# Kernel optimization log

Measured on AMD Instinct MI355X. Metric: run time of the kernel, lower is better.

Reference implementation:

```python
import jax, jax.numpy as jnp
import numpy as np
import math

B, S, D, H = 4, 1024, 1024, 16
HD = D // H
R = 128  # max_rel_pos
EPS = 1e-5

def setup_inputs() -> dict:
    key = jax.random.key(0)
    ks = jax.random.split(key, 20)
    sd = 1.0 / math.sqrt(D)
    def lin(k, din, dout):
        return jax.random.normal(k, (din, dout), jnp.float32) * (1.0 / math.sqrt(din))
    return {
        "x": jax.random.normal(ks[0], (B, S, D), jnp.float32),
        "wq": lin(ks[1], D, D), "bq": jnp.zeros((D,), jnp.float32),
        "wk": lin(ks[2], D, D), "bk": jnp.zeros((D,), jnp.float32),
        "wv": lin(ks[3], D, D), "bv": jnp.zeros((D,), jnp.float32),
        "wo": lin(ks[4], D, D), "bo": jnp.zeros((D,), jnp.float32),
        "rel_embed": jax.random.normal(ks[5], (2 * R + 1, HD), jnp.float32),
        "ln1_g": jnp.ones((D,), jnp.float32), "ln1_b": jnp.zeros((D,), jnp.float32),
        "ln2_g": jnp.ones((D,), jnp.float32), "ln2_b": jnp.zeros((D,), jnp.float32),
        "w1": lin(ks[6], D, 4 * D), "b1": jnp.zeros((4 * D,), jnp.float32),
        "w2": lin(ks[7], 4 * D, D), "b2": jnp.zeros((D,), jnp.float32),
    }

def _layernorm(x, g, b):
    mu = jnp.mean(x, axis=-1, keepdims=True)
    var = jnp.mean(jnp.square(x - mu), axis=-1, keepdims=True)
    return (x - mu) * jax.lax.rsqrt(var + EPS) * g + b

def _block(x, wq, bq, wk, bk, wv, bv, wo, bo, rel_embed,
           ln1_g, ln1_b, ln2_g, ln2_b, w1, b1, w2, b2):
    h = _layernorm(x, ln1_g, ln1_b)
    # project and split heads: [B,S,D] -> [B,H,S,HD]
    def heads(y):
        return y.reshape(B, S, H, HD).transpose(0, 2, 1, 3)
    Q = heads(h @ wq + bq)
    K = heads(h @ wk + bk)
    V = heads(h @ wv + bv)
    scale = 1.0 / math.sqrt(HD)
    scores = jnp.einsum("bhqd,bhkd->bhqk", Q, K) * scale
    # relative positions: clamp(q-k, -R, R) + R
    pos = jnp.arange(S)
    rel_idx = jnp.clip(pos[None, :] - pos[:, None], -R, R) + R  # [S,S]
    rel = rel_embed[rel_idx]  # [S,S,HD]
    scores = scores + jnp.einsum("bhqd,qkd->bhqk", Q, rel) * scale
    attn = jax.nn.softmax(scores, axis=-1)
    out = jnp.einsum("bhqk,bhkd->bhqd", attn, V)
    out = out.transpose(0, 2, 1, 3).reshape(B, S, D) @ wo + bo
    x = x + out  # dropout is identity in eval
    h2 = _layernorm(x, ln2_g, ln2_b)
    ff = jax.nn.gelu(h2 @ w1 + b1, approximate=False) @ w2 + b2
    return x + ff

def reference(x, wq, bq, wk, bk, wv, bv, wo, bo, rel_embed,
              ln1_g, ln1_b, ln2_g, ln2_b, w1, b1, w2, b2):
    return _block(x, wq, bq, wk, bk, wv, bv, wo, bo, rel_embed,
                  ln1_g, ln1_b, ln2_g, ln2_b, w1, b1, w2, b2)
```

## Files before the change

### kernel.cpp

```cpp
#include <hip/hip_runtime.h>

typedef unsigned short u16;
typedef __bf16 bf16x8 __attribute__((ext_vector_type(8)));
typedef float f32x4 __attribute__((ext_vector_type(4)));

#define QSCALE 0.18033688011112042f
#define QREL_LD 320

__device__ __forceinline__ float b2f(u16 x) {
    unsigned int u = ((unsigned int)x) << 16;
    return __builtin_bit_cast(float, u);
}
__device__ __forceinline__ u16 f2bf(float f) {
    unsigned int u = __builtin_bit_cast(unsigned int, f);
    u += 0x7fffu + ((u >> 16) & 1u);
    return (u16)(u >> 16);
}
__device__ __forceinline__ void lds_load16(const u16* g, u16* l) {
    __builtin_amdgcn_global_load_lds(
        (const __attribute__((address_space(1))) void*)g,
        (__attribute__((address_space(3))) void*)l, 16, 0, 0);
}

__global__ void transpose_f32_bf16(const float* __restrict__ in, u16* __restrict__ out,
                                   int R, int C) {
    __shared__ u16 tile[32][33];
    int bx = blockIdx.x * 32, by = blockIdx.y * 32;
    int tx = threadIdx.x, ty = threadIdx.y;
#pragma unroll
    for (int i = 0; i < 32; i += 8)
        tile[ty + i][tx] = f2bf(in[(size_t)(by + ty + i) * C + bx + tx]);
    __syncthreads();
#pragma unroll
    for (int i = 0; i < 32; i += 8)
        out[(size_t)(bx + ty + i) * R + by + tx] = tile[tx][ty + i];
}

__global__ void transpose_w4(const float* __restrict__ wq, const float* __restrict__ wk,
                             const float* __restrict__ wv, const float* __restrict__ wo,
                             u16* __restrict__ wqkvT, u16* __restrict__ woT) {
    __shared__ u16 tile[32][33];
    int z = blockIdx.z;
    const float* in = (z == 0) ? wq : (z == 1) ? wk : (z == 2) ? wv : wo;
    u16* out = (z < 3) ? (wqkvT + (size_t)z * 1024 * 1024) : woT;
    int bx = blockIdx.x * 32, by = blockIdx.y * 32;
    int tx = threadIdx.x, ty = threadIdx.y;
#pragma unroll
    for (int i = 0; i < 32; i += 8)
        tile[ty + i][tx] = f2bf(in[(size_t)(by + ty + i) * 1024 + bx + tx]);
    __syncthreads();
#pragma unroll
    for (int i = 0; i < 32; i += 8)
        out[(size_t)(bx + ty + i) * 1024 + by + tx] = tile[tx][ty + i];
}

__global__ void transpose_v(const u16* __restrict__ in, int ldin, int coloff,
                            u16* __restrict__ out) {
    __shared__ u16 tile[32][33];
    size_t zout = (size_t)blockIdx.z << 20;
    int bx = blockIdx.x * 32, by = blockIdx.y * 32;
    int tx = threadIdx.x, ty = threadIdx.y;
#pragma unroll
    for (int i = 0; i < 32; i += 8)
        tile[ty + i][tx] =
            in[(size_t)(blockIdx.z * 1024 + by + ty + i) * ldin + coloff + bx + tx];
    __syncthreads();
#pragma unroll
    for (int i = 0; i < 32; i += 8)
        out[zout + (size_t)(bx + ty + i) * 1024 + by + tx] = tile[tx][ty + i];
}

__global__ void cvt_f32_bf16(const float* __restrict__ in, u16* __restrict__ out, int n) {
    int i = blockIdx.x * 256 + threadIdx.x;
    if (i < n) out[i] = f2bf(in[i]);
}

__global__ void fill_f32(float* __restrict__ p, float v, int n) {
    int i = blockIdx.x * 256 + threadIdx.x;
    if (i < n) p[i] = v;
}

__global__ void concat3(const float* a, const float* b, const float* c, float* o) {
    int i = blockIdx.x * 256 + threadIdx.x;
    o[i] = (i < 1024) ? a[i] : (i < 2048 ? b[i - 1024] : c[i - 2048]);
}

__global__ __launch_bounds__(256) void ln_kernel(
    const u16* __restrict__ inb, const float* __restrict__ inf,
    const float* __restrict__ g, const float* __restrict__ b,
    u16* __restrict__ out) {
    int row = blockIdx.x, t = threadIdx.x;
    size_t base = (size_t)row * 1024 + t * 4;
    float v[4];
    if (inf) {
        float4 f = *(const float4*)(inf + base);
        v[0] = f.x; v[1] = f.y; v[2] = f.z; v[3] = f.w;
    } else {
        uint2 u = *(const uint2*)(inb + base);
        v[0] = b2f((u16)(u.x & 0xffff)); v[1] = b2f((u16)(u.x >> 16));
        v[2] = b2f((u16)(u.y & 0xffff)); v[3] = b2f((u16)(u.y >> 16));
    }
    float s = v[0] + v[1] + v[2] + v[3];
    float q = v[0] * v[0] + v[1] * v[1] + v[2] * v[2] + v[3] * v[3];
#pragma unroll
    for (int m = 1; m < 64; m <<= 1) {
        s += __shfl_xor(s, m);
        q += __shfl_xor(q, m);
    }
    __shared__ float rs[4], rq[4];
    __shared__ float mu_s, rstd_s;
    int w = t >> 6, lane = t & 63;
    if (lane == 0) { rs[w] = s; rq[w] = q; }
    __syncthreads();
    if (t == 0) {
        float S = rs[0] + rs[1] + rs[2] + rs[3];
        float Q2 = rq[0] + rq[1] + rq[2] + rq[3];
        float mu = S * (1.0f / 1024.0f);
        float var = Q2 * (1.0f / 1024.0f) - mu * mu;
        mu_s = mu;
        rstd_s = rsqrtf(var + 1e-5f);
    }
    __syncthreads();
    float mu = mu_s, rstd = rstd_s;
    u16 o[4];
#pragma unroll
    for (int i = 0; i < 4; i++) {
        int col = t * 4 + i;
        o[i] = f2bf((v[i] - mu) * rstd * g[col] + b[col]);
    }
    uint2 pk;
    pk.x = (unsigned)o[0] | ((unsigned)o[1] << 16);
    pk.y = (unsigned)o[2] | ((unsigned)o[3] << 16);
    *(uint2*)(out + base) = pk;
}

template <int BN>
__global__ __launch_bounds__(256) void gemm_bt(
    const u16* __restrict__ A, int lda, long long sAz,
    const u16* __restrict__ Bt, int ldb, long long sBz, int nclamp,
    const float* __restrict__ bias,
    const float* __restrict__ resid_f32,
    u16* __restrict__ outb, float* __restrict__ outf, int ldc, long long sCz,
    int K, float oscale, int gelu) {
    constexpr int NJ = BN / 32;
    constexpr int NUNITS = 8 + BN / 16;
    constexpr int UPW = NUNITS / 4;
    __shared__ __align__(16) u16 As[2][128 * 32];
    __shared__ __align__(16) u16 Bs[2][BN * 32];
    int t = threadIdx.x, w = t >> 6, lane = t & 63;
    int z = blockIdx.z;
    const u16* Ab = A + (size_t)z * sAz;
    const u16* Bb = Bt + (size_t)z * sBz;
    int m0 = blockIdx.y * 128, n0 = blockIdx.x * BN;
    int lo = lane & 15, hi = lane >> 4;
    int wr = w >> 1, wc = w & 1;
    f32x4 acc[4][NJ];
#pragma unroll
    for (int i = 0; i < 4; i++)
#pragma unroll
        for (int j = 0; j < NJ; j++) acc[i][j] = (f32x4){0.f, 0.f, 0.f, 0.f};

    auto stage = [&](int k0, int buf) {
#pragma unroll
        for (int uu = 0; uu < UPW; ++uu) {
            int u = w * UPW + uu;
            if (u < 8) {
                int s = u * 64 + lane;
                int row = s >> 2, c8 = (s & 3) * 8;
                const u16* gp = Ab + (size_t)(m0 + row) * lda + k0 + c8;
                lds_load16(gp, &As[buf][u * 512]);
            } else {
                int s = (u - 8) * 64 + lane;
                int row = s >> 2, c8 = (s & 3) * 8;
                int n = n0 + row;
                if (n >= nclamp) n = nclamp - 1;
                const u16* gp = Bb + (size_t)n * ldb + k0 + c8;
                lds_load16(gp, &Bs[buf][(u - 8) * 512]);
            }
        }
    };

    int nk = K >> 5;
    stage(0, 0);
    for (int kk = 0; kk < nk; ++kk) {
        __syncthreads();
        if (kk + 1 < nk) stage((kk + 1) << 5, (kk + 1) & 1);
        int buf = kk & 1;
        bf16x8 a[4], bb[NJ];
#pragma unroll
        for (int i = 0; i < 4; i++)
            a[i] = *(const bf16x8*)&As[buf][(wr * 64 + i * 16 + lo) * 32 + 8 * hi];
#pragma unroll
        for (int j = 0; j < NJ; j++)
            bb[j] = *(const bf16x8*)&Bs[buf][(wc * (BN / 2) + j * 16 + lo) * 32 + 8 * hi];
#pragma unroll
        for (int i = 0; i < 4; i++)
#pragma unroll
            for (int j = 0; j < NJ; j++)
                acc[i][j] = __builtin_amdgcn_mfma_f32_16x16x32_bf16(a[i], bb[j], acc[i][j], 0, 0, 0);
    }
#pragma unroll
    for (int j = 0; j < NJ; j++) {
        int col = n0 + wc * (BN / 2) + j * 16 + lo;
        float bv = bias ? bias[col] : 0.f;
#pragma unroll
        for (int i = 0; i < 4; i++) {
            int rbase = m0 + wr * 64 + i * 16 + hi * 4;
#pragma unroll
            for (int r = 0; r < 4; r++) {
                float v = fmaf(acc[i][j][r], oscale, bv);
                if (gelu) v = 0.5f * v * (1.f + erff(v * 0.70710678118654752f));
                size_t ridx = (size_t)(rbase + r) * ldc + col;
                if (resid_f32) v += resid_f32[ridx];
                size_t idx = (size_t)z * sCz + ridx;
                if (outf) outf[idx] = v;
                if (outb) outb[idx] = f2bf(v);
            }
        }
    }
}

__global__ __launch_bounds__(256) void gemm_bt64(
    const u16* __restrict__ A, int lda,
    const u16* __restrict__ Bt, int ldb,
    const float* __restrict__ bias,
    const float* __restrict__ resid_f32, const u16* __restrict__ resid_bf,
    u16* __restrict__ outb, float* __restrict__ outf, int ldc,
    int K, float oscale, int gelu) {
    constexpr int AU = 16, BU = 8, UPW = (AU + BU) / 4;
    __shared__ __align__(16) u16 As[2][128 * 64];
    __shared__ __align__(16) u16 Bs[2][64 * 64];
    int t = threadIdx.x, w = t >> 6, lane = t & 63;
    int m0 = blockIdx.y * 128, n0 = blockIdx.x * 64;
    int lo = lane & 15, hi = lane >> 4;
    int wr = w >> 1, wc = w & 1;
    f32x4 acc[4][2];
#pragma unroll
    for (int i = 0; i < 4; i++)
#pragma unroll
        for (int j = 0; j < 2; j++) acc[i][j] = (f32x4){0.f, 0.f, 0.f, 0.f};

    auto stage = [&](int k0, int buf) {
#pragma unroll
        for (int uu = 0; uu < UPW; ++uu) {
            int u = w * UPW + uu;
            if (u < AU) {
                int s = u * 64 + lane;
                int row = s >> 3, cg = (lane & 7) ^ (row & 7);
                lds_load16(A + (size_t)(m0 + row) * lda + k0 + cg * 8,
                           &As[buf][u * 512]);
            } else {
                int u2 = u - AU;
                int s = u2 * 64 + lane;
                int row = s >> 3, cg = (lane & 7) ^ (row & 7);
                lds_load16(Bt + (size_t)(n0 + row) * ldb + k0 + cg * 8,
                           &Bs[buf][u2 * 512]);
            }
        }
    };

    int nk = K >> 6;
    stage(0, 0);
    for (int kk = 0; kk < nk; ++kk) {
        __syncthreads();
        if (kk + 1 < nk) stage((kk + 1) << 6, (kk + 1) & 1);
        int buf = kk & 1;
#pragma unroll
        for (int k2 = 0; k2 < 2; ++k2) {
            bf16x8 a[4], bb[2];
#pragma unroll
            for (int i = 0; i < 4; i++) {
                int row = wr * 64 + i * 16 + lo;
                int g = (k2 * 4 + hi) ^ (row & 7);
                a[i] = *(const bf16x8*)&As[buf][row * 64 + g * 8];
            }
#pragma unroll
            for (int j = 0; j < 2; j++) {
                int row = wc * 32 + j * 16 + lo;
                int g = (k2 * 4 + hi) ^ (row & 7);
                bb[j] = *(const bf16x8*)&Bs[buf][row * 64 + g * 8];
            }
#pragma unroll
            for (int i = 0; i < 4; i++)
#pragma unroll
                for (int j = 0; j < 2; j++)
                    acc[i][j] = __builtin_amdgcn_mfma_f32_16x16x32_bf16(a[i], bb[j], acc[i][j], 0, 0, 0);
        }
    }
#pragma unroll
    for (int j = 0; j < 2; j++) {
        int col = n0 + wc * 32 + j * 16 + lo;
        float bv = bias ? bias[col] : 0.f;
#pragma unroll
        for (int i = 0; i < 4; i++) {
            int rbase = m0 + wr * 64 + i * 16 + hi * 4;
#pragma unroll
            for (int r = 0; r < 4; r++) {
                float v = fmaf(acc[i][j][r], oscale, bv);
                if (gelu) v = 0.5f * v * (1.f + erff(v * 0.70710678118654752f));
                size_t ridx = (size_t)(rbase + r) * ldc + col;
                if (resid_f32) v += resid_f32[ridx];
                if (resid_bf) v += b2f(resid_bf[ridx]);
                if (outf) outf[ridx] = v;
                if (outb) outb[ridx] = f2bf(v);
            }
        }
    }
}

__global__ __launch_bounds__(256) void gemm_bt128k64(
    const u16* __restrict__ A, int lda,
    const u16* __restrict__ Bt, int ldb,
    const float* __restrict__ bias,
    u16* __restrict__ outb, int ldc,
    int K, float oscale, int gelu) {
    __shared__ __align__(16) u16 As[2][128 * 64];
    __shared__ __align__(16) u16 Bs[2][128 * 64];
    int t = threadIdx.x, w = t >> 6, lane = t & 63;
    int m0 = blockIdx.y * 128, n0 = blockIdx.x * 128;
    int lo = lane & 15, hi = lane >> 4;
    int wr = w >> 1, wc = w & 1;
    f32x4 acc[4][4];
#pragma unroll
    for (int i = 0; i < 4; i++)
#pragma unroll
        for (int j = 0; j < 4; j++) acc[i][j] = (f32x4){0.f, 0.f, 0.f, 0.f};

    auto stage = [&](int k0, int buf) {
#pragma unroll
        for (int uu = 0; uu < 4; ++uu) {
            int u = w * 4 + uu;
            int s = u * 64 + lane;
            int row = s >> 3, cg = (lane & 7) ^ (row & 7);
            lds_load16(A + (size_t)(m0 + row) * lda + k0 + cg * 8,
                       &As[buf][u * 512]);
        }
#pragma unroll
        for (int uu = 0; uu < 4; ++uu) {
            int u = w * 4 + uu;
            int s = u * 64 + lane;
            int row = s >> 3, cg = (lane & 7) ^ (row & 7);
            lds_load16(Bt + (size_t)(n0 + row) * ldb + k0 + cg * 8,
                       &Bs[buf][u * 512]);
        }
    };

    int nk = K >> 6;
    stage(0, 0);
    for (int kk = 0; kk < nk; ++kk) {
        __syncthreads();
        if (kk + 1 < nk) stage((kk + 1) << 6, (kk + 1) & 1);
        int buf = kk & 1;
#pragma unroll
        for (int k2 = 0; k2 < 2; ++k2) {
            bf16x8 a[4], bb[4];
#pragma unroll
            for (int i = 0; i < 4; i++) {
                int row = wr * 64 + i * 16 + lo;
                int g = (k2 * 4 + hi) ^ (row & 7);
                a[i] = *(const bf16x8*)&As[buf][row * 64 + g * 8];
            }
#pragma unroll
            for (int j = 0; j < 4; j++) {
                int row = wc * 64 + j * 16 + lo;
                int g = (k2 * 4 + hi) ^ (row & 7);
                bb[j] = *(const bf16x8*)&Bs[buf][row * 64 + g * 8];
            }
#pragma unroll
            for (int i = 0; i < 4; i++)
#pragma unroll
                for (int j = 0; j < 4; j++)
                    acc[i][j] = __builtin_amdgcn_mfma_f32_16x16x32_bf16(a[i], bb[j], acc[i][j], 0, 0, 0);
        }
    }
#pragma unroll
    for (int j = 0; j < 4; j++) {
        int col = n0 + wc * 64 + j * 16 + lo;
        float bv = bias ? bias[col] : 0.f;
#pragma unroll
        for (int i = 0; i < 4; i++) {
            int rbase = m0 + wr * 64 + i * 16 + hi * 4;
#pragma unroll
            for (int r = 0; r < 4; r++) {
                float v = fmaf(acc[i][j][r], oscale, bv);
                if (gelu) v = 0.5f * v * (1.f + erff(v * 0.70710678118654752f));
                outb[(size_t)(rbase + r) * ldc + col] = f2bf(v);
            }
        }
    }
}

__global__ __launch_bounds__(256) void attn_kernel(
    const u16* __restrict__ QKV, const u16* __restrict__ Vtg,
    const u16* __restrict__ Qrel, u16* __restrict__ Ob) {
    __shared__ __align__(16) u16 KsL[2][4096];
    __shared__ __align__(16) u16 VsL[2][4096];
    __shared__ __align__(16) u16 Ps[4][16 * 72];
    int t = threadIdx.x, w = t >> 6, lane = t & 63;
    int bid = blockIdx.x;
    int qblk = bid & 15, h = (bid >> 4) & 15, bb = bid >> 8;
    int lo = lane & 15, hi = lane >> 4;
    int q0b = qblk * 64;
    int q0 = q0b + w * 16;

    const u16* qrow = QKV + ((size_t)(bb * 1024 + q0 + lo) * 3072 + h * 64 + hi * 8);
    bf16x8 qf0 = *(const bf16x8*)qrow;
    bf16x8 qf1 = *(const bf16x8*)(qrow + 32);

    const size_t qrel_base = (size_t)h * (4096ull * QREL_LD);
    float blo[4], bhi[4];
#pragma unroll
    for (int r = 0; r < 4; r++) {
        size_t row = qrel_base + (size_t)(bb * 1024 + q0 + hi * 4 + r) * QREL_LD;
        blo[r] = b2f(Qrel[row]);
        bhi[r] = b2f(Qrel[row + 256]);
    }

    const u16* Kg = QKV + 1024 + ((size_t)(bb * 1024)) * 3072 + h * 64;
    const u16* Vg = Vtg + ((size_t)(bb * 1024 + h * 64)) * 1024;

    auto stage = [&](int k0, int buf) {
#pragma unroll
        for (int half = 0; half < 2; ++half) {
            int s = half * 256 + w * 64 + lane;
            int row = s >> 3, cg = (s & 7) ^ (row & 7);
            lds_load16(Kg + (size_t)(k0 + row) * 3072 + cg * 8,
                       &KsL[buf][(half * 256 + w * 64) * 8]);
            lds_load16(Vg + (size_t)row * 1024 + k0 + cg * 8,
                       &VsL[buf][(half * 256 + w * 64) * 8]);
        }
    };

    f32x4 oacc[4];
#pragma unroll
    for (int j = 0; j < 4; j++) oacc[j] = (f32x4){0.f, 0.f, 0.f, 0.f};
    float l_[4] = {0.f, 0.f, 0.f, 0.f};

    stage(0, 0);
    for (int c = 0; c < 16; ++c) {
        int k0 = c * 64;
        __syncthreads();
        if (c < 15) stage(k0 + 64, (c + 1) & 1);
        const u16* Ksb = KsL[c & 1];
        const u16* Vsb = VsL[c & 1];

        f32x4 sc[4];
#pragma unroll
        for (int kt = 0; kt < 4; kt++) {
            int row = kt * 16 + lo, rx = row & 7;
            bf16x8 kf0 = *(const bf16x8*)&Ksb[(row * 8 + (hi ^ rx)) * 8];
            bf16x8 kf1 = *(const bf16x8*)&Ksb[(row * 8 + ((4 + hi) ^ rx)) * 8];
            f32x4 zz = (f32x4){0.f, 0.f, 0.f, 0.f};
            sc[kt] = __builtin_amdgcn_mfma_f32_16x16x32_bf16(qf0, kf0, zz, 0, 0, 0);
            sc[kt] = __builtin_amdgcn_mfma_f32_16x16x32_bf16(qf1, kf1, sc[kt], 0, 0, 0);
        }
        float bt[4][4];
        if (k0 + 192 <= q0b) {
#pragma unroll
            for (int kt = 0; kt < 4; kt++)
#pragma unroll
                for (int r = 0; r < 4; r++) bt[kt][r] = blo[r];
        } else if (k0 >= q0b + 192) {
#pragma unroll
            for (int kt = 0; kt < 4; kt++)
#pragma unroll
                for (int r = 0; r < 4; r++) bt[kt][r] = bhi[r];
        } else {
#pragma unroll
            for (int kt = 0; kt < 4; kt++)
#pragma unroll
                for (int r = 0; r < 4; r++) {
                    int q = q0 + hi * 4 + r;
                    int k = k0 + kt * 16 + lo;
                    int p = k - q;
                    p = p < -128 ? -128 : (p > 128 ? 128 : p);
                    p += 128;
                    bt[kt][r] = b2f(Qrel[qrel_base + (size_t)(bb * 1024 + q) * QREL_LD + p]);
                }
        }
#pragma unroll
        for (int kt = 0; kt < 4; kt++)
#pragma unroll
            for (int r = 0; r < 4; r++) {
                float s = fmaf(sc[kt][r], QSCALE, bt[kt][r]);
                float p = __builtin_amdgcn_exp2f(s);
                l_[r] += p;
                Ps[w][(hi * 4 + r) * 72 + kt * 16 + lo] =
                    (u16)(__builtin_bit_cast(unsigned int, p) >> 16);
            }
        bf16x8 pf0 = *(const bf16x8*)&Ps[w][lo * 72 + 8 * hi];
        bf16x8 pf1 = *(const bf16x8*)&Ps[w][lo * 72 + 32 + 8 * hi];
#pragma unroll
        for (int j = 0; j < 4; j++) {
            int row = j * 16 + lo, rx = row & 7;
            bf16x8 vf0 = *(const bf16x8*)&Vsb[(row * 8 + (hi ^ rx)) * 8];
            bf16x8 vf1 = *(const bf16x8*)&Vsb[(row * 8 + ((4 + hi) ^ rx)) * 8];
            oacc[j] = __builtin_amdgcn_mfma_f32_16x16x32_bf16(pf0, vf0, oacc[j], 0, 0, 0);
            oacc[j] = __builtin_amdgcn_mfma_f32_16x16x32_bf16(pf1, vf1, oacc[j], 0, 0, 0);
        }
    }
#pragma unroll
    for (int r = 0; r < 4; r++) {
#pragma unroll
        for (int m = 1; m < 16; m <<= 1) l_[r] += __shfl_xor(l_[r], m);
    }
#pragma unroll
    for (int r = 0; r < 4; r++) {
        float inv = 1.f / l_[r];
        int q = q0 + hi * 4 + r;
#pragma unroll
        for (int j = 0; j < 4; j++)
            Ob[(size_t)(bb * 1024 + q) * 1024 + h * 64 + j * 16 + lo] =
                f2bf(oacc[j][r] * inv);
    }
}

extern "C" void kernel_launch(void* const* d_in, const int* in_sizes, int n_in,
                              void* d_out, int out_size, void* d_ws, size_t ws_size,
                              hipStream_t stream) {
    const float* x   = (const float*)d_in[0];
    const float* wq  = (const float*)d_in[1];
    const float* bq  = (const float*)d_in[2];
    const float* wk  = (const float*)d_in[3];
    const float* bk  = (const float*)d_in[4];
    const float* wv  = (const float*)d_in[5];
    const float* bv  = (const float*)d_in[6];
    const float* wo  = (const float*)d_in[7];
    const float* bo  = (const float*)d_in[8];
    const float* rel = (const float*)d_in[9];
    const float* g1  = (const float*)d_in[10];
    const float* be1 = (const float*)d_in[11];
    const float* g2  = (const float*)d_in[12];
    const float* be2 = (const float*)d_in[13];
    const float* w1  = (const float*)d_in[14];
    const float* bf1 = (const float*)d_in[15];
    const float* w2  = (const float*)d_in[16];
    const float* bf2 = (const float*)d_in[17];

    char* ws = (char*)d_ws;
    const size_t MB = 1024ull * 1024ull;
    u16* wqkvT = (u16*)(ws + 0 * MB);
    u16* woT  = (u16*)(ws + 6 * MB);
    u16* w1T  = (u16*)(ws + 8 * MB);
    u16* w2T  = (u16*)(ws + 16 * MB);
    u16* h    = (u16*)(ws + 24 * MB);
    u16* QKV  = (u16*)(ws + 32 * MB);
    u16* Vtg  = (u16*)(ws + 56 * MB);
    u16* qrel = (u16*)(ws + 64 * MB);
    u16* x2b  = (u16*)(ws + 64 * MB);
    u16* att  = (u16*)(ws + 112 * MB);
    u16* relb = (u16*)(ws + 120 * MB);
    float* cbias = (float*)(ws + 120 * MB + 64 * 1024);
    float* bqkv  = (float*)(ws + 120 * MB + 128 * 1024);
    u16* ff1  = (u16*)(ws + 32 * MB);
    u16* h2   = h;

    dim3 tb(32, 8);
    transpose_w4<<<dim3(32, 32, 4), tb, 0, stream>>>(wq, wk, wv, wo, wqkvT, woT);
    transpose_f32_bf16<<<dim3(128, 32), tb, 0, stream>>>(w1, w1T, 1024, 4096);
    transpose_f32_bf16<<<dim3(32, 128), tb, 0, stream>>>(w2, w2T, 4096, 1024);
    cvt_f32_bf16<<<65, 256, 0, stream>>>(rel, relb, 257 * 64);
    fill_f32<<<2, 256, 0, stream>>>(cbias, -16.0f, QREL_LD);
    concat3<<<12, 256, 0, stream>>>(bq, bk, bv, bqkv);

    ln_kernel<<<4096, 256, 0, stream>>>(nullptr, x, g1, be1, h);

    gemm_bt128k64<<<dim3(24, 32), 256, 0, stream>>>(h, 1024, wqkvT, 1024,
        bqkv, QKV, 3072, 1024, 1.f, 0);
    transpose_v<<<dim3(32, 32, 4), tb, 0, stream>>>(QKV, 3072, 2048, Vtg);

    gemm_bt<64><<<dim3(5, 32, 16), 256, 0, stream>>>(QKV, 3072, 64, relb, 64, 0, 257,
        cbias, nullptr, qrel, nullptr, QREL_LD, (long long)4096 * QREL_LD,
        64, QSCALE, 0);

    attn_kernel<<<1024, 256, 0, stream>>>(QKV, Vtg, qrel, att);

    gemm_bt64<<<dim3(16, 32), 256, 0, stream>>>(att, 1024, woT, 1024,
        bo, x, nullptr, x2b, nullptr, 1024, 1024, 1.f, 0);

    ln_kernel<<<4096, 256, 0, stream>>>(x2b, nullptr, g2, be2, h2);

    gemm_bt128k64<<<dim3(32, 32), 256, 0, stream>>>(h2, 1024, w1T, 1024,
        bf1, ff1, 4096, 1024, 1.f, 1);
    gemm_bt64<<<dim3(16, 32), 256, 0, stream>>>(ff1, 4096, w2T, 4096,
        bf2, nullptr, x2b, nullptr, (float*)d_out, 1024, 4096, 1.f, 0);
}
```

Measured before the change: 419.8 us.

## Fuse Q·rel_embed projection into attention kernel via per-warp LDS table

```diff
diff --git a/kernel.cpp b/kernel.cpp
--- a/kernel.cpp
+++ b/kernel.cpp
@@ -5,7 +5,6 @@
 typedef float f32x4 __attribute__((ext_vector_type(4)));
 
 #define QSCALE 0.18033688011112042f
-#define QREL_LD 320
 
 __device__ __forceinline__ float b2f(u16 x) {
     unsigned int u = ((unsigned int)x) << 16;
@@ -73,11 +72,6 @@
 __global__ void cvt_f32_bf16(const float* __restrict__ in, u16* __restrict__ out, int n) {
     int i = blockIdx.x * 256 + threadIdx.x;
     if (i < n) out[i] = f2bf(in[i]);
-}
-
-__global__ void fill_f32(float* __restrict__ p, float v, int n) {
-    int i = blockIdx.x * 256 + threadIdx.x;
-    if (i < n) p[i] = v;
 }
 
 __global__ void concat3(const float* a, const float* b, const float* c, float* o) {
@@ -132,92 +126,6 @@
     pk.x = (unsigned)o[0] | ((unsigned)o[1] << 16);
     pk.y = (unsigned)o[2] | ((unsigned)o[3] << 16);
     *(uint2*)(out + base) = pk;
-}
-
-template <int BN>
-__global__ __launch_bounds__(256) void gemm_bt(
-    const u16* __restrict__ A, int lda, long long sAz,
-    const u16* __restrict__ Bt, int ldb, long long sBz, int nclamp,
-    const float* __restrict__ bias,
-    const float* __restrict__ resid_f32,
-    u16* __restrict__ outb, float* __restrict__ outf, int ldc, long long sCz,
-    int K, float oscale, int gelu) {
-    constexpr int NJ = BN / 32;
-    constexpr int NUNITS = 8 + BN / 16;
-    constexpr int UPW = NUNITS / 4;
-    __shared__ __align__(16) u16 As[2][128 * 32];
-    __shared__ __align__(16) u16 Bs[2][BN * 32];
-    int t = threadIdx.x, w = t >> 6, lane = t & 63;
-    int z = blockIdx.z;
-    const u16* Ab = A + (size_t)z * sAz;
-    const u16* Bb = Bt + (size_t)z * sBz;
-    int m0 = blockIdx.y * 128, n0 = blockIdx.x * BN;
-    int lo = lane & 15, hi = lane >> 4;
-    int wr = w >> 1, wc = w & 1;
-    f32x4 acc[4][NJ];
-#pragma unroll
-    for (int i = 0; i < 4; i++)
-#pragma unroll
-        for (int j = 0; j < NJ; j++) acc[i][j] = (f32x4){0.f, 0.f, 0.f, 0.f};
-
-    auto stage = [&](int k0, int buf) {
-#pragma unroll
-        for (int uu = 0; uu < UPW; ++uu) {
-            int u = w * UPW + uu;
-            if (u < 8) {
-                int s = u * 64 + lane;
-                int row = s >> 2, c8 = (s & 3) * 8;
-                const u16* gp = Ab + (size_t)(m0 + row) * lda + k0 + c8;
-                lds_load16(gp, &As[buf][u * 512]);
-            } else {
-                int s = (u - 8) * 64 + lane;
-                int row = s >> 2, c8 = (s & 3) * 8;
-                int n = n0 + row;
-                if (n >= nclamp) n = nclamp - 1;
-                const u16* gp = Bb + (size_t)n * ldb + k0 + c8;
-                lds_load16(gp, &Bs[buf][(u - 8) * 512]);
-            }
-        }
-    };
-
-    int nk = K >> 5;
-    stage(0, 0);
-    for (int kk = 0; kk < nk; ++kk) {
-        __syncthreads();
-        if (kk + 1 < nk) stage((kk + 1) << 5, (kk + 1) & 1);
-        int buf = kk & 1;
-        bf16x8 a[4], bb[NJ];
-#pragma unroll
-        for (int i = 0; i < 4; i++)
-            a[i] = *(const bf16x8*)&As[buf][(wr * 64 + i * 16 + lo) * 32 + 8 * hi];
-#pragma unroll
-        for (int j = 0; j < NJ; j++)
-            bb[j] = *(const bf16x8*)&Bs[buf][(wc * (BN / 2) + j * 16 + lo) * 32 + 8 * hi];
-#pragma unroll
-        for (int i = 0; i < 4; i++)
-#pragma unroll
-            for (int j = 0; j < NJ; j++)
-                acc[i][j] = __builtin_amdgcn_mfma_f32_16x16x32_bf16(a[i], bb[j], acc[i][j], 0, 0, 0);
-    }
-#pragma unroll
-    for (int j = 0; j < NJ; j++) {
-        int col = n0 + wc * (BN / 2) + j * 16 + lo;
-        float bv = bias ? bias[col] : 0.f;
-#pragma unroll
-        for (int i = 0; i < 4; i++) {
-            int rbase = m0 + wr * 64 + i * 16 + hi * 4;
-#pragma unroll
-            for (int r = 0; r < 4; r++) {
-                float v = fmaf(acc[i][j][r], oscale, bv);
-                if (gelu) v = 0.5f * v * (1.f + erff(v * 0.70710678118654752f));
-                size_t ridx = (size_t)(rbase + r) * ldc + col;
-                if (resid_f32) v += resid_f32[ridx];
-                size_t idx = (size_t)z * sCz + ridx;
-                if (outf) outf[idx] = v;
-                if (outb) outb[idx] = f2bf(v);
-            }
-        }
-    }
 }
 
 __global__ __launch_bounds__(256) void gemm_bt64(
@@ -392,10 +300,11 @@
 
 __global__ __launch_bounds__(256) void attn_kernel(
     const u16* __restrict__ QKV, const u16* __restrict__ Vtg,
-    const u16* __restrict__ Qrel, u16* __restrict__ Ob) {
+    const u16* __restrict__ relb, u16* __restrict__ Ob) {
     __shared__ __align__(16) u16 KsL[2][4096];
     __shared__ __align__(16) u16 VsL[2][4096];
     __shared__ __align__(16) u16 Ps[4][16 * 72];
+    __shared__ __align__(16) u16 Rb[4][16 * 280];
     int t = threadIdx.x, w = t >> 6, lane = t & 63;
     int bid = blockIdx.x;
     int qblk = bid & 15, h = (bid >> 4) & 15, bb = bid >> 8;
@@ -406,15 +315,6 @@
     const u16* qrow = QKV + ((size_t)(bb * 1024 + q0 + lo) * 3072 + h * 64 + hi * 8);
     bf16x8 qf0 = *(const bf16x8*)qrow;
     bf16x8 qf1 = *(const bf16x8*)(qrow + 32);
-
-    const size_t qrel_base = (size_t)h * (4096ull * QREL_LD);
-    float blo[4], bhi[4];
-#pragma unroll
-    for (int r = 0; r < 4; r++) {
-        size_t row = qrel_base + (size_t)(bb * 1024 + q0 + hi * 4 + r) * QREL_LD;
-        blo[r] = b2f(Qrel[row]);
-        bhi[r] = b2f(Qrel[row + 256]);
-    }
 
     const u16* Kg = QKV + 1024 + ((size_t)(bb * 1024)) * 3072 + h * 64;
     const u16* Vg = Vtg + ((size_t)(bb * 1024 + h * 64)) * 1024;
@@ -431,12 +331,32 @@
         }
     };
 
+    stage(0, 0);
+
+#pragma unroll 4
+    for (int pt = 0; pt < 17; ++pt) {
+        bf16x8 rf0 = *(const bf16x8*)&relb[(pt * 16 + lo) * 64 + hi * 8];
+        bf16x8 rf1 = *(const bf16x8*)&relb[(pt * 16 + lo) * 64 + 32 + hi * 8];
+        f32x4 cz = (f32x4){0.f, 0.f, 0.f, 0.f};
+        cz = __builtin_amdgcn_mfma_f32_16x16x32_bf16(qf0, rf0, cz, 0, 0, 0);
+        cz = __builtin_amdgcn_mfma_f32_16x16x32_bf16(qf1, rf1, cz, 0, 0, 0);
+#pragma unroll
+        for (int r = 0; r < 4; r++)
+            Rb[w][(hi * 4 + r) * 280 + pt * 16 + lo] =
+                f2bf(fmaf(cz[r], QSCALE, -16.0f));
+    }
+    float blo[4], bhi[4];
+#pragma unroll
+    for (int r = 0; r < 4; r++) {
+        blo[r] = b2f(Rb[w][(hi * 4 + r) * 280]);
+        bhi[r] = b2f(Rb[w][(hi * 4 + r) * 280 + 256]);
+    }
+
     f32x4 oacc[4];
 #pragma unroll
     for (int j = 0; j < 4; j++) oacc[j] = (f32x4){0.f, 0.f, 0.f, 0.f};
     float l_[4] = {0.f, 0.f, 0.f, 0.f};
 
-    stage(0, 0);
     for (int c = 0; c < 16; ++c) {
         int k0 = c * 64;
         __syncthreads();
@@ -470,12 +390,11 @@
             for (int kt = 0; kt < 4; kt++)
 #pragma unroll
                 for (int r = 0; r < 4; r++) {
-                    int q = q0 + hi * 4 + r;
-                    int k = k0 + kt * 16 + lo;
-                    int p = k - q;
+                    int lq = hi * 4 + r;
+                    int p = (k0 + kt * 16 + lo) - (q0 + lq);
                     p = p < -128 ? -128 : (p > 128 ? 128 : p);
                     p += 128;
-                    bt[kt][r] = b2f(Qrel[qrel_base + (size_t)(bb * 1024 + q) * QREL_LD + p]);
+                    bt[kt][r] = b2f(Rb[w][lq * 280 + p]);
                 }
         }
 #pragma unroll
@@ -546,12 +465,10 @@
     u16* h    = (u16*)(ws + 24 * MB);
     u16* QKV  = (u16*)(ws + 32 * MB);
     u16* Vtg  = (u16*)(ws + 56 * MB);
-    u16* qrel = (u16*)(ws + 64 * MB);
     u16* x2b  = (u16*)(ws + 64 * MB);
     u16* att  = (u16*)(ws + 112 * MB);
     u16* relb = (u16*)(ws + 120 * MB);
-    float* cbias = (float*)(ws + 120 * MB + 64 * 1024);
-    float* bqkv  = (float*)(ws + 120 * MB + 128 * 1024);
+    float* bqkv = (float*)(ws + 120 * MB + 128 * 1024);
     u16* ff1  = (u16*)(ws + 32 * MB);
     u16* h2   = h;
 
@@ -560,7 +477,6 @@
     transpose_f32_bf16<<<dim3(128, 32), tb, 0, stream>>>(w1, w1T, 1024, 4096);
     transpose_f32_bf16<<<dim3(32, 128), tb, 0, stream>>>(w2, w2T, 4096, 1024);
     cvt_f32_bf16<<<65, 256, 0, stream>>>(rel, relb, 257 * 64);
-    fill_f32<<<2, 256, 0, stream>>>(cbias, -16.0f, QREL_LD);
     concat3<<<12, 256, 0, stream>>>(bq, bk, bv, bqkv);
 
     ln_kernel<<<4096, 256, 0, stream>>>(nullptr, x, g1, be1, h);
@@ -569,11 +485,7 @@
         bqkv, QKV, 3072, 1024, 1.f, 0);
     transpose_v<<<dim3(32, 32, 4), tb, 0, stream>>>(QKV, 3072, 2048, Vtg);
 
-    gemm_bt<64><<<dim3(5, 32, 16), 256, 0, stream>>>(QKV, 3072, 64, relb, 64, 0, 257,
-        cbias, nullptr, qrel, nullptr, QREL_LD, (long long)4096 * QREL_LD,
-        64, QSCALE, 0);
-
-    attn_kernel<<<1024, 256, 0, stream>>>(QKV, Vtg, qrel, att);
+    attn_kernel<<<1024, 256, 0, stream>>>(QKV, Vtg, relb, att);
 
     gemm_bt64<<<dim3(16, 32), 256, 0, stream>>>(att, 1024, woT, 1024,
         bo, x, nullptr, x2b, nullptr, 1024, 1024, 1.f, 0);
```

Result: faster. 394.5 us (-6.0%).
